# Optimization experiments

Hardware: AMD Instinct MI355X
Metric: run time of the kernel (lower is better)

## Reference

```python
import jax, jax.numpy as jnp
import numpy as np

K = 11            # kernel size
D = K * K         # flow input size = 121
HID = 15          # MADE hidden size
NB = 5            # n_blocks
ALPHA = 1e-6      # post_process inverse-logit alpha
EPS = 1e-5        # BatchNorm eps
SCALE = 2         # 1/scale_factor
LOG2PI = float(np.log(2.0 * np.pi))


def _degrees(block):
    # MAF flips input ordering between successive MADE blocks
    d = jnp.arange(D)
    return d if block % 2 == 0 else d[::-1]


def _masks(deg_in):
    # MADE masks: hidden degrees = arange(HID) % (D-1)
    dh = jnp.arange(HID) % (D - 1)
    m1 = (dh[:, None] >= deg_in[None, :]).astype(jnp.float32)   # [HID, D]
    m2 = (deg_in[:, None] > dh[None, :]).astype(jnp.float32)    # [D, HID] (strict for output)
    m2 = jnp.concatenate([m2, m2], axis=0)                      # [2D, HID] (m and loga share mask)
    return m1, m2


def _made_inverse(u, W1, b1, W2, b2, deg):
    m1, m2 = _masks(deg)
    Wm1 = (W1 * m1).T   # [D, HID]
    Wm2 = (W2 * m2).T   # [HID, 2D]

    def net(x):
        h = jax.nn.relu(x @ Wm1 + b1)
        out = h @ Wm2 + b2
        return out[:, :D], out[:, D:]

    def step(x, i):
        m, loga = net(x)
        x = x.at[:, i].set(u[:, i] * jnp.exp(loga[:, i]) + m[:, i])
        return x, None

    x, _ = jax.lax.scan(step, jnp.zeros_like(u), deg)
    # so evaluating on fully-filled x equals the torch loop's last-iteration loga
    _, loga = net(x)
    return x, loga


def _flow_inverse(u, W1, b1, W2, b2, bn_log_gamma, bn_beta, bn_mean, bn_var):
    # FlowSequential.inverse: iterate blocks in reverse, each block = [MADE, BatchNorm]
    x = u
    sum_ldj = jnp.zeros_like(u)
    for b in reversed(range(NB)):
        # BatchNorm inverse (eval mode, running stats)
        var, mean = bn_var[b], bn_mean[b]
        lg, beta = bn_log_gamma[b], bn_beta[b]
        x = (x - beta) * jnp.exp(-lg) * jnp.sqrt(var + EPS) + mean
        sum_ldj = sum_ldj + (0.5 * jnp.log(var + EPS) - lg)[None, :]
        # MADE inverse
        x, loga = _made_inverse(x, W1[b], b1[b], W2[b], b2[b], _degrees(b))
        sum_ldj = sum_ldj + loga
    return x, sum_ldj


def _post_process(x):
    x = (jax.nn.sigmoid(x) - ALPHA) / (1.0 - 2.0 * ALPHA)
    x = x / jnp.sum(x, axis=1, keepdims=True)   # kernel sums to 1
    return x.reshape(x.shape[0], 1, K, K)


def setup_inputs() -> dict:
    key = jax.random.key(0)
    ks = jax.random.split(key, 10)
    s = 0.1
    return {
        "input_tensor": jax.random.normal(ks[0], (1, 3, 4096, 4096), jnp.float32),
        "kernel_code": jax.random.normal(ks[1], (1, D), jnp.float32),
        "W1": jax.random.normal(ks[2], (NB, HID, D), jnp.float32) * s,
        "b1": jax.random.normal(ks[3], (NB, HID), jnp.float32) * s,
        "W2": jax.random.normal(ks[4], (NB, 2 * D, HID), jnp.float32) * s,
        "b2": jax.random.normal(ks[5], (NB, 2 * D), jnp.float32) * s,
        "bn_log_gamma": jax.random.normal(ks[6], (NB, D), jnp.float32) * s,
        "bn_beta": jax.random.normal(ks[7], (NB, D), jnp.float32) * s,
        "bn_mean": jax.random.normal(ks[8], (NB, D), jnp.float32) * s,
        "bn_var": jax.random.uniform(ks[9], (NB, D), jnp.float32) * 0.5 + 0.5,
    }


def reference(input_tensor, kernel_code, W1, b1, W2, b2, bn_log_gamma, bn_beta, bn_mean, bn_var):
    # kp.inverse: flow inverse + log prob under base dist
    x, sum_ldj = _flow_inverse(kernel_code, W1, b1, W2, b2, bn_log_gamma, bn_beta, bn_mean, bn_var)
    base_lp = jnp.sum(-0.5 * kernel_code**2 - 0.5 * LOG2PI, axis=1)
    logprob = base_lp - jnp.sum(sum_ldj, axis=1)   # (unused downstream, kept for fidelity)
    out_k = _post_process(x)                        # [1,1,K,K]
    # grouped conv + stride-2 subsample: conv-with-stride == full conv then [0::2] slice
    w = jnp.broadcast_to(out_k, (3, 1, K, K))
    out_put = jax.lax.conv_general_dilated(
        input_tensor, w, window_strides=(SCALE, SCALE), padding='VALID',
        dimension_numbers=('NCHW', 'OIHW', 'NCHW'), feature_group_count=3)
    return out_put, out_k[0, 0]
```

## Files before the change

### kernel.cpp

```cpp
#include <hip/hip_runtime.h>

#define DD   121
#define NHID 15
#define NBLK 5
#define KS   11
#define IW   4096
#define OW   2043

#define ROR_ADD(v, N)                                                         \
  v += __int_as_float(__builtin_amdgcn_update_dpp(                            \
      0, __float_as_int(v), 0x120 + (N), 0xF, 0xF, true))

__device__ __forceinline__ void stage_weights(
    float* W1d, float* W2d, float* b2d, float* b1d,
    const float* __restrict__ W1, const float* __restrict__ W2,
    const float* __restrict__ b2, const float* __restrict__ b1,
    int blk, int t0, int nt)
{
    const float* W1b = W1 + blk * NHID * DD;
    const float* W2b = W2 + blk * 2 * DD * NHID;
    const float* b2b = b2 + blk * 2 * DD;
    for (int i = t0; i < NHID * DD; i += nt) W1d[i] = W1b[i];
    for (int k = t0; k < DD * NHID; k += nt) {
        const int idx = k / NHID, j = k - idx * NHID;
        W2d[idx*32 + 2*j]     = W2b[idx*NHID + j];
        W2d[idx*32 + 2*j + 1] = W2b[(DD + idx)*NHID + j];
    }
    for (int i = t0; i < DD; i += nt) {
        W2d[i*32 + 30] = 0.f;
        W2d[i*32 + 31] = 0.f;
        b2d[2*i]     = b2b[i];
        b2d[2*i + 1] = b2b[DD + i];
    }
    for (int i = t0; i < NHID; i += nt) b1d[i] = b1[blk*NHID + i];
}

__global__ __launch_bounds__(128) void flow_kernel(
    const float* __restrict__ kc,
    const float* __restrict__ W1, const float* __restrict__ b1,
    const float* __restrict__ W2, const float* __restrict__ b2,
    const float* __restrict__ lg, const float* __restrict__ beta,
    const float* __restrict__ mean, const float* __restrict__ var,
    float* __restrict__ kout)
{
    __shared__ float xs[DD];
    __shared__ float us[DD];
    __shared__ float W1s[2][NHID * DD];
    __shared__ float W2p[2][DD * 32];
    __shared__ float b2p[2][DD * 2];
    __shared__ float b1s[2][16];

    const int tid  = threadIdx.x;
    const int wv   = tid >> 6;
    const int lane = tid & 63;

    stage_weights(W1s[0], W2p[0], b2p[0], b1s[0], W1, W2, b2, b1, NBLK - 1, tid, 128);
    if (tid < DD) xs[tid] = kc[tid];
    __syncthreads();

    for (int b = NBLK - 1; b >= 0; --b) {
        const int buf = (NBLK - 1 - b) & 1;
        if (wv == 1) {
            if (b > 0)
                stage_weights(W1s[buf^1], W2p[buf^1], b2p[buf^1], b1s[buf^1],
                              W1, W2, b2, b1, b - 1, lane, 64);
        } else {
            for (int i = lane; i < DD; i += 64) {
                float s = sqrtf(var[b*DD + i] + 1e-5f);
                us[i] = (xs[i] - beta[b*DD + i]) * __expf(-lg[b*DD + i]) * s + mean[b*DD + i];
            }
            const int evenb = ((b & 1) == 0);
            if (lane < 16) {
                const int j  = lane;
                const int jc = (j < NHID) ? j : (NHID - 1);
                float pre_h = (j < NHID) ? b1s[buf][j] : 0.f;

                auto step = [&](int t, int iS, float2 wpS, float w1S, float uvS, float2 bpS) {
                    float h  = (j < t && j < NHID) ? fmaxf(pre_h, 0.f) : 0.f;
                    float pm = h * wpS.x;
                    float pa = h * wpS.y;
                    ROR_ADD(pm, 1); ROR_ADD(pa, 1);
                    ROR_ADD(pm, 2); ROR_ADD(pa, 2);
                    ROR_ADD(pm, 4); ROR_ADD(pa, 4);
                    ROR_ADD(pm, 8); ROR_ADD(pa, 8);
                    const float xv = fmaf(uvS, __expf(pa + bpS.y), pm + bpS.x);
                    if (j >= t && j < NHID) pre_h = fmaf(xv, w1S, pre_h);
                    if (j == 0) xs[iS] = xv;
                };

                int iA, iB, iC, iD;
                float2 wpA, wpB, wpC, wpD, bpA, bpB, bpC, bpD;
                float  w1A, w1B, w1C, w1D, uvA, uvB, uvC, uvD;

                #define PRELOAD(S, T) { const int tt = (T);                                 \
                    i##S  = evenb ? tt : (DD - 1 - tt);                                     \
                    wp##S = *(const float2*)&W2p[buf][i##S*32 + 2*j];                       \
                    w1##S = W1s[buf][jc*DD + i##S];                                         \
                    uv##S = us[i##S];                                                       \
                    bp##S = *(const float2*)&b2p[buf][2*i##S]; }

                #define QSTEP(S, TCUR, TNEXT) {                                             \
                    int tt = (TNEXT); if (tt > DD - 1) tt = DD - 1;                         \
                    const int ip = evenb ? tt : (DD - 1 - tt);                              \
                    const float2 wpN = *(const float2*)&W2p[buf][ip*32 + 2*j];              \
                    const float  w1N = W1s[buf][jc*DD + ip];                                \
                    const float  uvN = us[ip];                                              \
                    const float2 bpN = *(const float2*)&b2p[buf][2*ip];                     \
                    step((TCUR), i##S, wp##S, w1##S, uv##S, bp##S);                         \
                    i##S = ip; wp##S = wpN; w1##S = w1N; uv##S = uvN; bp##S = bpN; }

                PRELOAD(A, 0) PRELOAD(B, 1) PRELOAD(C, 2) PRELOAD(D, 3)
                #pragma unroll 1
                for (int it = 0; it < 30; ++it) {
                    QSTEP(A, 4*it + 0, 4*it + 4)
                    QSTEP(B, 4*it + 1, 4*it + 5)
                    QSTEP(C, 4*it + 2, 4*it + 6)
                    QSTEP(D, 4*it + 3, 4*it + 7)
                }
                step(DD - 1, iA, wpA, w1A, uvA, bpA);
                #undef PRELOAD
                #undef QSTEP
            }
        }
        __syncthreads();
    }

    if (tid < 64) {
        const float A = 1e-6f;
        float y0, y1 = 0.f;
        {
            float v = xs[tid];
            y0 = (1.f / (1.f + __expf(-v)) - A) / (1.f - 2.f*A);
        }
        if (tid + 64 < DD) {
            float v = xs[tid + 64];
            y1 = (1.f / (1.f + __expf(-v)) - A) / (1.f - 2.f*A);
        }
        float s = y0 + y1;
        #pragma unroll
        for (int off = 32; off >= 1; off >>= 1) s += __shfl_xor(s, off, 64);
        kout[tid] = y0 / s;
        if (tid + 64 < DD) kout[tid + 64] = y1 / s;
    }
}

#define CTY 25
#define CSE 264

__global__ __launch_bounds__(256) void conv_kernel(
    const float* __restrict__ in, const float* __restrict__ kf,
    float* __restrict__ out)
{
    __shared__ __align__(16) float E[CTY * CSE];
    __shared__ __align__(16) float O[CTY * CSE];

    const int tid = threadIdx.x;
    const int cch = blockIdx.z;
    const int ox0 = blockIdx.x * 256;
    const int oy0 = blockIdx.y * 8;
    const int gx0 = ox0 * 2;
    const int gy0 = oy0 * 2;

    const float* __restrict__ inc = in + (size_t)cch * IW * IW;

    {
        const int l = tid & 31;
        for (int r = tid >> 5; r < CTY; r += 8) {
            const int gy = gy0 + r;
            const bool rowok = (gy < IW);
            const float* rowp = inc + (size_t)gy * IW + gx0;
            for (int c = l; c < 130; c += 32) {
                float4 g = make_float4(0.f, 0.f, 0.f, 0.f);
                if (rowok) {
                    if (gx0 + 4*c + 3 < IW) {
                        g = *(const float4*)(rowp + 4*c);
                    } else {
                        float t0 = (gx0 + 4*c + 0 < IW) ? rowp[4*c + 0] : 0.f;
                        float t1 = (gx0 + 4*c + 1 < IW) ? rowp[4*c + 1] : 0.f;
                        float t2 = (gx0 + 4*c + 2 < IW) ? rowp[4*c + 2] : 0.f;
                        float t3 = (gx0 + 4*c + 3 < IW) ? rowp[4*c + 3] : 0.f;
                        g = make_float4(t0, t1, t2, t3);
                    }
                }
                *(float2*)&E[r*CSE + 2*c] = make_float2(g.x, g.z);
                *(float2*)&O[r*CSE + 2*c] = make_float2(g.y, g.w);
            }
            if (l == 0) {
                float v = 0.f;
                if (rowok && (gx0 + 520) < IW) v = rowp[520];
                E[r*CSE + 260] = v;
            }
        }
    }
    __syncthreads();

    const int w = tid >> 6;
    const int l = tid & 63;

    float acc[2][4] = {{0.f,0.f,0.f,0.f},{0.f,0.f,0.f,0.f}};

    #pragma unroll 1
    for (int rw = 0; rw < 13; ++rw) {
        const int row = 4*w + rw;
        const float* Er = &E[row*CSE + 4*l];
        const float* Or = &O[row*CSE + 4*l];
        const float4 ea = *(const float4*)(Er);
        const float4 eb = *(const float4*)(Er + 4);
        const float4 ex = *(const float4*)(Er + 8);
        const float4 oa = *(const float4*)(Or);
        const float4 ob = *(const float4*)(Or + 4);
        const float ev[9] = {ea.x,ea.y,ea.z,ea.w,eb.x,eb.y,eb.z,eb.w,ex.x};
        const float ov[8] = {oa.x,oa.y,oa.z,oa.w,ob.x,ob.y,ob.z,ob.w};
        #pragma unroll
        for (int q = 0; q < 2; ++q) {
            const int ky = rw - 2*q;
            if (ky < 0 || ky > 10) continue;
            #pragma unroll
            for (int m = 0; m < 6; ++m) {
                const float we = kf[ky*KS + 2*m];
                #pragma unroll
                for (int j = 0; j < 4; ++j)
                    acc[q][j] = fmaf(ev[m + j], we, acc[q][j]);
            }
            #pragma unroll
            for (int m = 0; m < 5; ++m) {
                const float wo = kf[ky*KS + 2*m + 1];
                #pragma unroll
                for (int j = 0; j < 4; ++j)
                    acc[q][j] = fmaf(ov[m + j], wo, acc[q][j]);
            }
        }
    }

    const bool okx = (ox0 + 255) < OW;
    #pragma unroll
    for (int q = 0; q < 2; ++q) {
        const int oy = oy0 + 2*w + q;
        if (oy >= OW) continue;
        const size_t base = ((size_t)cch * OW + oy) * OW;
        if (okx) {
            #pragma unroll
            for (int j = 0; j < 4; ++j)
                out[base + ox0 + 4*l + j] = acc[q][j];
        } else {
            #pragma unroll
            for (int j = 0; j < 4; ++j) {
                const int ox = ox0 + 4*l + j;
                if (ox < OW) out[base + ox] = acc[q][j];
            }
        }
    }
}

extern "C" void kernel_launch(void* const* d_in, const int* in_sizes, int n_in,
                              void* d_out, int out_size, void* d_ws, size_t ws_size,
                              hipStream_t stream)
{
    const float* in   = (const float*)d_in[0];
    const float* kc   = (const float*)d_in[1];
    const float* W1   = (const float*)d_in[2];
    const float* b1   = (const float*)d_in[3];
    const float* W2   = (const float*)d_in[4];
    const float* b2   = (const float*)d_in[5];
    const float* lg   = (const float*)d_in[6];
    const float* beta = (const float*)d_in[7];
    const float* mean = (const float*)d_in[8];
    const float* var  = (const float*)d_in[9];

    float* out  = (float*)d_out;
    float* kout = out + (size_t)3 * OW * OW;

    flow_kernel<<<dim3(1), dim3(128), 0, stream>>>(kc, W1, b1, W2, b2, lg, beta, mean, var, kout);

    dim3 grid((OW + 255) / 256, (OW + 7) / 8, 3);
    conv_kernel<<<grid, dim3(256), 0, stream>>>(in, kout, out);
}
```

Before: 218.1 us.

## Double conv block size to one output row per wave with register prefetch

The conv kernel now launches 512 threads per block, so each of the eight waves computes a single output row instead of two. The inner loop is restructured into a two-slot register double buffer that loads the next input row from shared memory while the current one is being accumulated. The intent is to put more waves in flight per compute unit for the same shared-memory tile, and to hide LDS latency behind the FMAs. The cost is more LDS reads per output, since each input row now feeds one output row instead of two.

```diff
diff --git a/kernel.cpp b/kernel.cpp
--- a/kernel.cpp
+++ b/kernel.cpp
@@ -147,7 +147,7 @@
 #define CTY 25
 #define CSE 264
 
-__global__ __launch_bounds__(256) void conv_kernel(
+__global__ __launch_bounds__(512) void conv_kernel(
     const float* __restrict__ in, const float* __restrict__ kf,
     float* __restrict__ out)
 {
@@ -164,12 +164,12 @@
     const float* __restrict__ inc = in + (size_t)cch * IW * IW;
 
     {
-        const int l = tid & 31;
-        for (int r = tid >> 5; r < CTY; r += 8) {
+        const int l = tid & 63;
+        for (int r = tid >> 6; r < CTY; r += 8) {
             const int gy = gy0 + r;
             const bool rowok = (gy < IW);
             const float* rowp = inc + (size_t)gy * IW + gx0;
-            for (int c = l; c < 130; c += 32) {
+            for (int c = l; c < 130; c += 64) {
                 float4 g = make_float4(0.f, 0.f, 0.f, 0.f);
                 if (rowok) {
                     if (gx0 + 4*c + 3 < IW) {
@@ -197,56 +197,66 @@
     const int w = tid >> 6;
     const int l = tid & 63;
 
-    float acc[2][4] = {{0.f,0.f,0.f,0.f},{0.f,0.f,0.f,0.f}};
-
+    float acc[4] = {0.f, 0.f, 0.f, 0.f};
+
+    float4 eaA, ebA, exA, oaA, obA;
+    float4 eaB, ebB, exB, oaB, obB;
+
+    #define LOADSLOT(S, KY) {                                                 \
+        int rr = 2*w + (KY); if (rr > CTY - 1) rr = CTY - 1;                  \
+        const float* Er = &E[rr*CSE + 4*l];                                   \
+        const float* Or = &O[rr*CSE + 4*l];                                   \
+        ea##S = *(const float4*)(Er);                                         \
+        eb##S = *(const float4*)(Er + 4);                                     \
+        ex##S = *(const float4*)(Er + 8);       \
+        oa##S = *(const float4*)(Or);                                         \
+        ob##S = *(const float4*)(Or + 4); }
+
+    #define COMP(S, KY) {                                                     \
+        const float ev[9] = {ea##S.x, ea##S.y, ea##S.z, ea##S.w,              \
+                             eb##S.x, eb##S.y, eb##S.z, eb##S.w, ex##S.x};    \
+        const float ov[8] = {oa##S.x, oa##S.y, oa##S.z, oa##S.w,              \
+                             ob##S.x, ob##S.y, ob##S.z, ob##S.w};             \
+        const float* kr = kf + (KY)*KS;                                       \
+        _Pragma("unroll")                                                     \
+        for (int m = 0; m < 6; ++m) {                                         \
+            const float we = kr[2*m];                                         \
+            _Pragma("unroll")                                                 \
+            for (int j = 0; j < 4; ++j) acc[j] = fmaf(ev[m+j], we, acc[j]);   \
+        }                                                                     \
+        _Pragma("unroll")                                                     \
+        for (int m = 0; m < 5; ++m) {                                         \
+            const float wo = kr[2*m + 1];                                     \
+            _Pragma("unroll")                                                 \
+            for (int j = 0; j < 4; ++j) acc[j] = fmaf(ov[m+j], wo, acc[j]);   \
+        } }
+
+    LOADSLOT(A, 0)
+    LOADSLOT(B, 1)
     #pragma unroll 1
-    for (int rw = 0; rw < 13; ++rw) {
-        const int row = 4*w + rw;
-        const float* Er = &E[row*CSE + 4*l];
-        const float* Or = &O[row*CSE + 4*l];
-        const float4 ea = *(const float4*)(Er);
-        const float4 eb = *(const float4*)(Er + 4);
-        const float4 ex = *(const float4*)(Er + 8);
-        const float4 oa = *(const float4*)(Or);
-        const float4 ob = *(const float4*)(Or + 4);
-        const float ev[9] = {ea.x,ea.y,ea.z,ea.w,eb.x,eb.y,eb.z,eb.w,ex.x};
-        const float ov[8] = {oa.x,oa.y,oa.z,oa.w,ob.x,ob.y,ob.z,ob.w};
-        #pragma unroll
-        for (int q = 0; q < 2; ++q) {
-            const int ky = rw - 2*q;
-            if (ky < 0 || ky > 10) continue;
-            #pragma unroll
-            for (int m = 0; m < 6; ++m) {
-                const float we = kf[ky*KS + 2*m];
-                #pragma unroll
-                for (int j = 0; j < 4; ++j)
-                    acc[q][j] = fmaf(ev[m + j], we, acc[q][j]);
-            }
-            #pragma unroll
-            for (int m = 0; m < 5; ++m) {
-                const float wo = kf[ky*KS + 2*m + 1];
-                #pragma unroll
-                for (int j = 0; j < 4; ++j)
-                    acc[q][j] = fmaf(ov[m + j], wo, acc[q][j]);
-            }
-        }
-    }
-
-    const bool okx = (ox0 + 255) < OW;
-    #pragma unroll
-    for (int q = 0; q < 2; ++q) {
-        const int oy = oy0 + 2*w + q;
-        if (oy >= OW) continue;
+    for (int it = 0; it < 5; ++it) {
+        const int ky = 2*it;
+        COMP(A, ky)
+        LOADSLOT(A, ky + 2)
+        COMP(B, ky + 1)
+        LOADSLOT(B, ky + 3)
+    }
+    COMP(A, 10)
+    #undef LOADSLOT
+    #undef COMP
+
+    const int oy = oy0 + w;
+    if (oy < OW) {
         const size_t base = ((size_t)cch * OW + oy) * OW;
-        if (okx) {
+        if ((ox0 + 255) < OW) {
             #pragma unroll
             for (int j = 0; j < 4; ++j)
-                out[base + ox0 + 4*l + j] = acc[q][j];
+                out[base + ox0 + 4*l + j] = acc[j];
         } else {
             #pragma unroll
             for (int j = 0; j < 4; ++j) {
                 const int ox = ox0 + 4*l + j;
-                if (ox < OW) out[base + ox] = acc[q][j];
+                if (ox < OW) out[base + ox] = acc[j];
             }
         }
     }
@@ -273,5 +283,5 @@
     flow_kernel<<<dim3(1), dim3(128), 0, stream>>>(kc, W1, b1, W2, b2, lg, beta, mean, var, kout);
 
     dim3 grid((OW + 255) / 256, (OW + 7) / 8, 3);
-    conv_kernel<<<grid, dim3(256), 0, stream>>>(in, kout, out);
-}
+    conv_kernel<<<grid, dim3(512), 0, stream>>>(in, kout, out);
+}
```

New measurement: 235.6 us. 8.0% more time.
